# Optimization experiments

Hardware: AMD Instinct MI355X
Metric: run time of the kernel (lower is better)

Reference implementation:

```python
import jax, jax.numpy as jnp
import numpy as np

N_HEAD = 12

def setup_inputs() -> dict:
    key = jax.random.key(0)
    ks = jax.random.split(key, 5)
    B, T, C = 4, 2048, 768
    x = jax.random.normal(ks[0], (B, T, C), dtype=jnp.float32)
    s_in = 1.0 / np.sqrt(C)
    W_qkv = jax.random.normal(ks[1], (C, 3 * C), dtype=jnp.float32) * s_in
    b_qkv = jnp.zeros((3 * C,), dtype=jnp.float32)
    W_proj = jax.random.normal(ks[2], (C, C), dtype=jnp.float32) * s_in
    b_proj = jnp.zeros((C,), dtype=jnp.float32)
    return {"x": x, "W_qkv": W_qkv, "b_qkv": b_qkv, "W_proj": W_proj, "b_proj": b_proj}


def reference(x, W_qkv, b_qkv, W_proj, b_proj):
    B, T, C = x.shape
    H = N_HEAD
    D = C // H  # head dim
    qkv = x @ W_qkv + b_qkv                      # [B,T,3C]
    q, k, v = jnp.split(qkv, 3, axis=-1)
    # [B,T,C] -> [B,H,T,D]
    q = q.reshape(B, T, H, D).transpose(0, 2, 1, 3)
    k = k.reshape(B, T, H, D).transpose(0, 2, 1, 3)
    v = v.reshape(B, T, H, D).transpose(0, 2, 1, 3)
    att = jnp.einsum("bhqd,bhkd->bhqk", q, k) / jnp.sqrt(jnp.asarray(D, x.dtype))
    causal = jnp.tril(jnp.ones((T, T), dtype=bool))
    att = jnp.where(causal, att, jnp.asarray(-jnp.inf, att.dtype))
    att = jax.nn.softmax(att, axis=-1)
    y = jnp.einsum("bhqk,bhkd->bhqd", att, v)    # [B,H,T,D]
    y = y.transpose(0, 2, 1, 3).reshape(B, T, C)
    return y @ W_proj + b_proj
```

## Files before the change

### kernel.cpp

```cpp
#include <hip/hip_runtime.h>
#include <hip/hip_bf16.h>

typedef __bf16 bf16x8 __attribute__((ext_vector_type(8)));
typedef float f32x4 __attribute__((ext_vector_type(4)));
typedef unsigned int u32x4 __attribute__((ext_vector_type(4)));
typedef unsigned int u32x2 __attribute__((ext_vector_type(2)));
typedef int i32x2 __attribute__((ext_vector_type(2)));
typedef unsigned short u16;
typedef unsigned long long u64;

#define WAITVM(n) asm volatile("s_waitcnt vmcnt(" #n ")" ::: "memory")
#define SBAR() asm volatile("s_barrier" ::: "memory")

__device__ __forceinline__ u16 f2bf(float f) {
  unsigned u = __builtin_bit_cast(unsigned, f);
  u += 0x7FFFu + ((u >> 16) & 1u);
  return (u16)(u >> 16);
}
__device__ __forceinline__ unsigned cvtpk(float a, float b) {
  float2 f; f.x = a; f.y = b;
  __hip_bfloat162 h = __float22bfloat162_rn(f);
  unsigned u;
  __builtin_memcpy(&u, &h, 4);
  return u;
}

__device__ __forceinline__ void plswap(unsigned &a, unsigned &b) {
  i32x2 r = __builtin_amdgcn_permlane32_swap((int)a, (int)b, false, false);
  a = (unsigned)r[0];
  b = (unsigned)r[1];
}

__device__ __forceinline__ void gll16(const u16* g, u16* l) {
  __builtin_amdgcn_global_load_lds(
      (const __attribute__((address_space(1))) unsigned int*)g,
      (__attribute__((address_space(3))) unsigned int*)l, 16, 0, 0);
}

__global__ void cast_x_kernel(const float* __restrict__ in, u16* __restrict__ out, int n4) {
  int i = blockIdx.x * blockDim.x + threadIdx.x;
  if (i >= n4) return;
  f32x4 v = *(const f32x4*)(in + (size_t)i * 4);
  u32x2 pk;
  pk[0] = cvtpk(v[0], v[1]);
  pk[1] = cvtpk(v[2], v[3]);
  *(u32x2*)(out + (size_t)i * 4) = pk;
}

__global__ void transpose_cast_kernel(const float* __restrict__ W, u16* __restrict__ WT, int K, int N) {
  __shared__ float tile[32][33];
  int c0 = blockIdx.x * 32, r0 = blockIdx.y * 32;
  int tx = threadIdx.x & 31, tg = threadIdx.x >> 5;
#pragma unroll
  for (int i = 0; i < 4; ++i) {
    int r = tg + i * 8;
    tile[r][tx] = W[(size_t)(r0 + r) * N + c0 + tx];
  }
  __syncthreads();
#pragma unroll
  for (int i = 0; i < 4; ++i) {
    int r = tg + i * 8;
    WT[(size_t)(c0 + r) * K + r0 + tx] = f2bf(tile[tx][r]);
  }
}

__global__ __launch_bounds__(256, 4) void gemm_qkv_kernel(
    const u16* __restrict__ A, const u16* __restrict__ BT, const float* __restrict__ bias,
    u16* __restrict__ Qb, u16* __restrict__ Kb, u16* __restrict__ Vt) {
  constexpr int K = 768;
  constexpr int NS = K / 32;
  __shared__ u16 Asm[2][128 * 32];
  __shared__ u16 Bsm[2][128 * 32];
  const int tid = threadIdx.x;
  const int w = tid >> 6, lane = tid & 63;
  const int l15 = lane & 15, quad = lane >> 4;
  const int srow = tid >> 2, scol = (tid & 3) * 8;
  const int m0 = blockIdx.y * 128, n0 = blockIdx.x * 128;
  const u16* Ag = A + (size_t)(m0 + srow) * K + scol;
  const u16* Bg = BT + (size_t)(n0 + srow) * K + scol;
  const int mw = (w >> 1) * 64, nw = (w & 1) * 64;
  f32x4 acc[4][4];
#pragma unroll
  for (int i = 0; i < 4; ++i)
#pragma unroll
    for (int j = 0; j < 4; ++j) acc[i][j] = {0.f, 0.f, 0.f, 0.f};

  auto STAGE = [&](int buf, int ks) {
    const u16* a = Ag + ks * 32;
    const u16* b = Bg + ks * 32;
#pragma unroll
    for (int rb = 0; rb < 2; ++rb) {
      gll16(a + (size_t)rb * 64 * K, &Asm[buf][(rb * 64 + w * 16) * 32]);
      gll16(b + (size_t)rb * 64 * K, &Bsm[buf][(rb * 64 + w * 16) * 32]);
    }
  };
  auto COMPUTE = [&](int buf) {
    bf16x8 af[4], bfj[4];
#pragma unroll
    for (int i = 0; i < 4; ++i) af[i] = *(const bf16x8*)&Asm[buf][(mw + i * 16 + l15) * 32 + quad * 8];
#pragma unroll
    for (int j = 0; j < 4; ++j) bfj[j] = *(const bf16x8*)&Bsm[buf][(nw + j * 16 + l15) * 32 + quad * 8];
#pragma unroll
    for (int i = 0; i < 4; ++i)
#pragma unroll
      for (int j = 0; j < 4; ++j)
        acc[i][j] = __builtin_amdgcn_mfma_f32_16x16x32_bf16(af[i], bfj[j], acc[i][j], 0, 0, 0);
  };

  STAGE(0, 0);
  for (int s = 0; s + 2 < NS; s += 2) {
    STAGE(1, s + 1); WAITVM(4); SBAR(); COMPUTE(0); SBAR();
    STAGE(0, s + 2); WAITVM(4); SBAR(); COMPUTE(1); SBAR();
  }
  STAGE(1, NS - 1); WAITVM(4); SBAR(); COMPUTE(0);
  WAITVM(0); SBAR(); COMPUTE(1);

  const int sec = blockIdx.x / 6;
  const int nbase = n0 - sec * 768;
#pragma unroll
  for (int j = 0; j < 4; ++j) {
    const int nloc = nbase + nw + j * 16 + l15;
    const float bv = bias[sec * 768 + nloc];
    const int h = nloc >> 6, d = nloc & 63;
#pragma unroll
    for (int i = 0; i < 4; ++i) {
      const int m = m0 + mw + i * 16 + quad * 4;
      const int bb = m >> 11, trow = m & 2047;
      if (sec == 2) {
        u32x2 pk;
        pk[0] = cvtpk(acc[i][j][0] + bv, acc[i][j][1] + bv);
        pk[1] = cvtpk(acc[i][j][2] + bv, acc[i][j][3] + bv);
        *(u32x2*)(Vt + (size_t)((bb * 12 + h) * 64 + d) * 2048 + trow) = pk;
      } else {
        u16* dst = (sec == 0) ? Qb : Kb;
        const float scl = (sec == 0) ? 0.125f * 1.44269504f : 1.0f;
#pragma unroll
        for (int r = 0; r < 4; ++r)
          dst[(size_t)((bb * 12 + h) * 2048 + trow + r) * 64 + d] = f2bf((acc[i][j][r] + bv) * scl);
      }
    }
  }
}

__global__ __launch_bounds__(256, 4) void gemm_proj_kernel(
    const u16* __restrict__ A, const u16* __restrict__ BT, const float* __restrict__ bias,
    float* __restrict__ out) {
  constexpr int K = 768;
  constexpr int NS = K / 32;
  __shared__ u16 Asm[2][64 * 32];
  __shared__ u16 Bsm[2][128 * 32];
  const int tid = threadIdx.x;
  const int w = tid >> 6, lane = tid & 63;
  const int l15 = lane & 15, quad = lane >> 4;
  const int srow = tid >> 2, scol = (tid & 3) * 8;
  const int m0 = blockIdx.y * 64, n0 = blockIdx.x * 128;
  const u16* Ag = A + (size_t)(m0 + srow) * K + scol;
  const u16* Bg = BT + (size_t)(n0 + srow) * K + scol;
  const int mw = (w >> 1) * 32, nw = (w & 1) * 64;
  f32x4 acc[2][4];
#pragma unroll
  for (int i = 0; i < 2; ++i)
#pragma unroll
    for (int j = 0; j < 4; ++j) acc[i][j] = {0.f, 0.f, 0.f, 0.f};

  auto STAGE = [&](int buf, int ks) {
    const u16* a = Ag + ks * 32;
    const u16* b = Bg + ks * 32;
    gll16(a, &Asm[buf][(w * 16) * 32]);
#pragma unroll
    for (int rb = 0; rb < 2; ++rb)
      gll16(b + (size_t)rb * 64 * K, &Bsm[buf][(rb * 64 + w * 16) * 32]);
  };
  auto COMPUTE = [&](int buf) {
    bf16x8 af[2], bfj[4];
#pragma unroll
    for (int i = 0; i < 2; ++i) af[i] = *(const bf16x8*)&Asm[buf][(mw + i * 16 + l15) * 32 + quad * 8];
#pragma unroll
    for (int j = 0; j < 4; ++j) bfj[j] = *(const bf16x8*)&Bsm[buf][(nw + j * 16 + l15) * 32 + quad * 8];
#pragma unroll
    for (int i = 0; i < 2; ++i)
#pragma unroll
      for (int j = 0; j < 4; ++j)
        acc[i][j] = __builtin_amdgcn_mfma_f32_16x16x32_bf16(af[i], bfj[j], acc[i][j], 0, 0, 0);
  };

  STAGE(0, 0);
  for (int s = 0; s + 2 < NS; s += 2) {
    STAGE(1, s + 1); WAITVM(3); SBAR(); COMPUTE(0); SBAR();
    STAGE(0, s + 2); WAITVM(3); SBAR(); COMPUTE(1); SBAR();
  }
  STAGE(1, NS - 1); WAITVM(3); SBAR(); COMPUTE(0);
  WAITVM(0); SBAR(); COMPUTE(1);

#pragma unroll
  for (int j = 0; j < 4; ++j) {
    const int n = n0 + nw + j * 16 + l15;
    const float bv = bias[n];
#pragma unroll
    for (int i = 0; i < 2; ++i) {
      const int m = m0 + mw + i * 16 + quad * 4;
#pragma unroll
      for (int r = 0; r < 4; ++r) out[(size_t)(m + r) * 768 + n] = acc[i][j][r] + bv;
    }
  }
}

__global__ __launch_bounds__(256) void attn_split_kernel(
    const u16* __restrict__ Qg, const u16* __restrict__ Kg, const u16* __restrict__ Vtg,
    u16* __restrict__ Yb, float* __restrict__ Opart, float* __restrict__ lpart) {
  constexpr int T = 2048, D = 64;
  constexpr int LDP = 72;
  constexpr float MBOUND = 20.0f;
  __shared__ u16 Ks[2][64 * LDP];
  __shared__ u16 VTs[2][64 * LDP];
  const int s = 79 - blockIdx.x;
  const int bh = blockIdx.y;
  int qt, c;
  if (s < 8) { qt = s; c = 0; }
  else if (s < 24) { qt = 8 + ((s - 8) >> 1); c = (s - 8) & 1; }
  else if (s < 48) { int u = s - 24; int q3 = u / 3; qt = 16 + q3; c = u - 3 * q3; }
  else { int u = s - 48; qt = 24 + (u >> 2); c = u & 3; }
  const int niter = min(8, qt + 1 - 8 * c);
  const int tid = threadIdx.x;
  const int w = tid >> 6, lane = tid & 63;
  const int l15 = lane & 15, quad = lane >> 4;
  const int srow = tid >> 2, scol = (tid & 3) * 16;
  const u16* Kp = Kg + (size_t)bh * T * D;
  const u16* VTp = Vtg + (size_t)bh * D * T;

  const int qq = qt * 64 + w * 16 + l15;
  const u16* qrow = Qg + ((size_t)bh * T + qq) * D;
  const bf16x8 qfa = *(const bf16x8*)(qrow + quad * 8);
  const bf16x8 qfb = *(const bf16x8*)(qrow + 32 + quad * 8);

  u32x4 onesw; onesw[0] = 0x3F803F80u; onesw[1] = 0x3F803F80u; onesw[2] = 0x3F803F80u; onesw[3] = 0x3F803F80u;
  const bf16x8 ones = __builtin_bit_cast(bf16x8, onesw);

  f32x4 o[4] = {{0,0,0,0},{0,0,0,0},{0,0,0,0},{0,0,0,0}};
  f32x4 lacc = {0.f, 0.f, 0.f, 0.f};

  u32x4 kA, kB, vA, vB;
  auto LOADT = [&](int kt) {
    const int k1 = kt * 64;
    kA = *(const u32x4*)(Kp + (size_t)(k1 + srow) * D + scol);
    kB = *(const u32x4*)(Kp + (size_t)(k1 + srow) * D + scol + 8);
    vA = *(const u32x4*)(VTp + (size_t)srow * T + k1 + scol);
    vB = *(const u32x4*)(VTp + (size_t)srow * T + k1 + scol + 8);
  };
  auto STORET = [&](int buf) {
    *(u32x4*)&Ks[buf][srow * LDP + scol] = kA;
    *(u32x4*)&Ks[buf][srow * LDP + scol + 8] = kB;
    u32x2 t0; t0[0] = vA[0]; t0[1] = vA[1];
    u32x2 t1; t1[0] = vA[2]; t1[1] = vA[3];
    u32x2 t2; t2[0] = vB[0]; t2[1] = vB[1];
    u32x2 t3; t3[0] = vB[2]; t3[1] = vB[3];
    *(u32x2*)&VTs[buf][srow * LDP + scol] = t0;
    *(u32x2*)&VTs[buf][srow * LDP + scol + 8] = t1;
    *(u32x2*)&VTs[buf][srow * LDP + scol + 4] = t2;
    *(u32x2*)&VTs[buf][srow * LDP + scol + 12] = t3;
  };

  LOADT(c * 8);
  STORET(0);
  if (niter > 1) LOADT(c * 8 + 1);
  __syncthreads();

  for (int j = 0; j < niter; ++j) {
    const int buf = j & 1;
    const int ktg = c * 8 + j;
    f32x4 sA[4];
#pragma unroll
    for (int t = 0; t < 4; ++t) sA[t] = {-MBOUND, -MBOUND, -MBOUND, -MBOUND};
    __builtin_amdgcn_s_setprio(1);
#pragma unroll
    for (int t = 0; t < 4; ++t) {
      const bf16x8 kf0 = *(const bf16x8*)&Ks[buf][(t * 16 + l15) * LDP + quad * 8];
      const bf16x8 kf1 = *(const bf16x8*)&Ks[buf][(t * 16 + l15) * LDP + 32 + quad * 8];
      sA[t] = __builtin_amdgcn_mfma_f32_16x16x32_bf16(kf0, qfa, sA[t], 0, 0, 0);
      sA[t] = __builtin_amdgcn_mfma_f32_16x16x32_bf16(kf1, qfb, sA[t], 0, 0, 0);
    }
    __builtin_amdgcn_s_setprio(0);
    if (ktg == qt) {
      const int k0 = ktg * 64;
#pragma unroll
      for (int t = 0; t < 4; ++t)
#pragma unroll
        for (int r = 0; r < 4; ++r)
          if (k0 + t * 16 + quad * 4 + r > qq) sA[t][r] = -1e30f;
    }
    unsigned W[4][2];
#pragma unroll
    for (int t = 0; t < 4; ++t) {
      float e0 = __builtin_amdgcn_exp2f(sA[t][0]);
      float e1 = __builtin_amdgcn_exp2f(sA[t][1]);
      float e2 = __builtin_amdgcn_exp2f(sA[t][2]);
      float e3 = __builtin_amdgcn_exp2f(sA[t][3]);
      W[t][0] = cvtpk(e0, e1);
      W[t][1] = cvtpk(e2, e3);
    }
    plswap(W[0][0], W[1][0]);
    plswap(W[0][1], W[1][1]);
    plswap(W[2][0], W[3][0]);
    plswap(W[2][1], W[3][1]);
    u32x4 paw; paw[0] = W[0][0]; paw[1] = W[0][1]; paw[2] = W[1][0]; paw[3] = W[1][1];
    u32x4 pbw; pbw[0] = W[2][0]; pbw[1] = W[2][1]; pbw[2] = W[3][0]; pbw[3] = W[3][1];
    const bf16x8 pa = __builtin_bit_cast(bf16x8, paw);
    const bf16x8 pb = __builtin_bit_cast(bf16x8, pbw);
    __builtin_amdgcn_s_setprio(1);
    lacc = __builtin_amdgcn_mfma_f32_16x16x32_bf16(ones, pa, lacc, 0, 0, 0);
    lacc = __builtin_amdgcn_mfma_f32_16x16x32_bf16(ones, pb, lacc, 0, 0, 0);
#pragma unroll
    for (int t = 0; t < 4; ++t) {
      const bf16x8 vf0 = *(const bf16x8*)&VTs[buf][(t * 16 + l15) * LDP + quad * 8];
      const bf16x8 vf1 = *(const bf16x8*)&VTs[buf][(t * 16 + l15) * LDP + 32 + quad * 8];
      o[t] = __builtin_amdgcn_mfma_f32_16x16x32_bf16(vf0, pa, o[t], 0, 0, 0);
      o[t] = __builtin_amdgcn_mfma_f32_16x16x32_bf16(vf1, pb, o[t], 0, 0, 0);
    }
    __builtin_amdgcn_s_setprio(0);
    if (j + 1 < niter) {
      STORET(buf ^ 1);
      if (j + 2 < niter) LOADT(c * 8 + j + 2);
    }
    __syncthreads();
  }

  const float lv = lacc[0];
  if (qt <= 7) {
    const float inv = 1.f / lv;
    const int bidx = bh / 12, hidx = bh % 12;
    u16* y = Yb + ((size_t)bidx * T + qq) * 768 + hidx * 64;
#pragma unroll
    for (int t = 0; t < 4; ++t) {
      u32x2 pk;
      pk[0] = cvtpk(o[t][0] * inv, o[t][1] * inv);
      pk[1] = cvtpk(o[t][2] * inv, o[t][3] * inv);
      *(u32x2*)(y + t * 16 + quad * 4) = pk;
    }
  } else {
    const size_t pidx = (size_t)bh * 80 + s;
    float* Op = Opart + pidx * 4096 + (size_t)(w * 16 + l15) * 64;
#pragma unroll
    for (int t = 0; t < 4; ++t) *(f32x4*)(Op + t * 16 + quad * 4) = o[t];
    if (quad == 0) lpart[pidx * 64 + w * 16 + l15] = lv;
  }
}

__global__ __launch_bounds__(256) void attn_combine_kernel(
    const float* __restrict__ Opart, const float* __restrict__ lpart, u16* __restrict__ Yb) {
  constexpr int T = 2048;
  const int qt = 8 + blockIdx.x;
  const int bh = blockIdx.y;
  const int nch = (qt < 16) ? 2 : (qt < 24) ? 3 : 4;
  const int off = (qt < 16) ? 8 + (qt - 8) * 2 : (qt < 24) ? 24 + (qt - 16) * 3 : 48 + (qt - 24) * 4;
  const size_t base = (size_t)bh * 80 + off;
  const int tid = threadIdx.x;
  const int q = tid >> 2, db = (tid & 3) * 16;
  f32x4 o[4] = {{0,0,0,0},{0,0,0,0},{0,0,0,0},{0,0,0,0}};
  float l = 0.f;
  for (int cc = 0; cc < nch; ++cc) {
    const float* Op = Opart + (base + cc) * 4096 + (size_t)q * 64 + db;
#pragma unroll
    for (int v = 0; v < 4; ++v) o[v] += *(const f32x4*)(Op + v * 4);
    l += lpart[(base + cc) * 64 + q];
  }
  const float inv = 1.f / l;
  const int bidx = bh / 12, hidx = bh % 12;
  u16* y = Yb + ((size_t)bidx * T + qt * 64 + q) * 768 + hidx * 64 + db;
  u32x4 pk;
  pk[0] = cvtpk(o[0][0] * inv, o[0][1] * inv);
  pk[1] = cvtpk(o[0][2] * inv, o[0][3] * inv);
  pk[2] = cvtpk(o[1][0] * inv, o[1][1] * inv);
  pk[3] = cvtpk(o[1][2] * inv, o[1][3] * inv);
  *(u32x4*)y = pk;
  pk[0] = cvtpk(o[2][0] * inv, o[2][1] * inv);
  pk[1] = cvtpk(o[2][2] * inv, o[2][3] * inv);
  pk[2] = cvtpk(o[3][0] * inv, o[3][1] * inv);
  pk[3] = cvtpk(o[3][2] * inv, o[3][3] * inv);
  *(u32x4*)(y + 8) = pk;
}

__global__ __launch_bounds__(256) void attn_kernel(
    const u16* __restrict__ Qg, const u16* __restrict__ Kg, const u16* __restrict__ Vtg,
    u16* __restrict__ Yb) {
  constexpr int T = 2048, D = 64;
  constexpr int LDP = 72;
  constexpr float MBOUND = 20.0f;
  __shared__ u16 Ks[64 * LDP];
  __shared__ u16 VTs[64 * LDP];
  __shared__ u16 Ps[4 * 32 * LDP];
  const int qb = 15 - blockIdx.x;
  const int bh = blockIdx.y;
  const int Q0 = qb * 128;
  const int bidx = bh / 12, hidx = bh % 12;
  const int tid = threadIdx.x;
  const int w = tid >> 6, lane = tid & 63;
  const int l15 = lane & 15, quad = lane >> 4;
  const int srow = tid >> 2, scol = (tid & 3) * 16;
  const u16* Kp = Kg + (size_t)bh * T * D;
  const u16* VTp = Vtg + (size_t)bh * D * T;
  u16* pw0 = &Ps[(w * 32) * LDP];
  u16* pw1 = &Ps[(w * 32 + 16) * LDP];
  const u16* qrow0 = Qg + ((size_t)bh * T + Q0 + w * 16 + l15) * D;
  const bf16x8 qf0a = *(const bf16x8*)(qrow0 + quad * 8);
  const bf16x8 qf0b = *(const bf16x8*)(qrow0 + 32 + quad * 8);
  const bf16x8 qf1a = *(const bf16x8*)(qrow0 + (size_t)64 * D + quad * 8);
  const bf16x8 qf1b = *(const bf16x8*)(qrow0 + (size_t)64 * D + 32 + quad * 8);
  const int qq0 = Q0 + w * 16 + l15, qq1 = qq0 + 64;
  f32x4 o0[4] = {{0,0,0,0},{0,0,0,0},{0,0,0,0},{0,0,0,0}};
  f32x4 o1[4] = {{0,0,0,0},{0,0,0,0},{0,0,0,0},{0,0,0,0}};
  float l0v = 0.f, l1v = 0.f;
  const int nkt = 2 * qb + 2;
  u32x4 kA = *(const u32x4*)(Kp + (size_t)srow * D + scol);
  u32x4 kB = *(const u32x4*)(Kp + (size_t)srow * D + scol + 8);
  u32x4 vA = *(const u32x4*)(VTp + (size_t)srow * T + scol);
  u32x4 vB = *(const u32x4*)(VTp + (size_t)srow * T + scol + 8);
  for (int kt = 0; kt < nkt; ++kt) {
    __syncthreads();
    *(u32x4*)&Ks[srow * LDP + scol] = kA;
    *(u32x4*)&Ks[srow * LDP + scol + 8] = kB;
    *(u32x4*)&VTs[srow * LDP + scol] = vA;
    *(u32x4*)&VTs[srow * LDP + scol + 8] = vB;
    __syncthreads();
    if (kt + 1 < nkt) {
      const int k1 = (kt + 1) * 64;
      kA = *(const u32x4*)(Kp + (size_t)(k1 + srow) * D + scol);
      kB = *(const u32x4*)(Kp + (size_t)(k1 + srow) * D + scol + 8);
      vA = *(const u32x4*)(VTp + (size_t)srow * T + k1 + scol);
      vB = *(const u32x4*)(VTp + (size_t)srow * T + k1 + scol + 8);
    }
    const int k0 = kt * 64;
    const bool g0a = (kt <= 2 * qb);
    f32x4 s0[4] = {{0,0,0,0},{0,0,0,0},{0,0,0,0},{0,0,0,0}};
    f32x4 s1[4] = {{0,0,0,0},{0,0,0,0},{0,0,0,0},{0,0,0,0}};
#pragma unroll
    for (int t = 0; t < 4; ++t) {
      const bf16x8 kf0 = *(const bf16x8*)&Ks[(t * 16 + l15) * LDP + quad * 8];
      const bf16x8 kf1 = *(const bf16x8*)&Ks[(t * 16 + l15) * LDP + 32 + quad * 8];
      s0[t] = __builtin_amdgcn_mfma_f32_16x16x32_bf16(kf0, qf0a, s0[t], 0, 0, 0);
      s0[t] = __builtin_amdgcn_mfma_f32_16x16x32_bf16(kf1, qf0b, s0[t], 0, 0, 0);
      s1[t] = __builtin_amdgcn_mfma_f32_16x16x32_bf16(kf0, qf1a, s1[t], 0, 0, 0);
      s1[t] = __builtin_amdgcn_mfma_f32_16x16x32_bf16(kf1, qf1b, s1[t], 0, 0, 0);
    }
    if (g0a) {
      if (kt == 2 * qb) {
#pragma unroll
        for (int t = 0; t < 4; ++t)
#pragma unroll
          for (int r = 0; r < 4; ++r)
            if (k0 + t * 16 + quad * 4 + r > qq0) s0[t][r] = -1e30f;
      }
#pragma unroll
      for (int t = 0; t < 4; ++t) {
        float e0 = __builtin_amdgcn_exp2f(s0[t][0] - MBOUND);
        float e1 = __builtin_amdgcn_exp2f(s0[t][1] - MBOUND);
        float e2 = __builtin_amdgcn_exp2f(s0[t][2] - MBOUND);
        float e3 = __builtin_amdgcn_exp2f(s0[t][3] - MBOUND);
        l0v += (e0 + e1) + (e2 + e3);
        u32x2 pk;
        pk[0] = cvtpk(e0, e1);
        pk[1] = cvtpk(e2, e3);
        *(u32x2*)&pw0[l15 * LDP + t * 16 + quad * 4] = pk;
      }
    }
    {
      if (kt == 2 * qb + 1) {
#pragma unroll
        for (int t = 0; t < 4; ++t)
#pragma unroll
          for (int r = 0; r < 4; ++r)
            if (k0 + t * 16 + quad * 4 + r > qq1) s1[t][r] = -1e30f;
      }
#pragma unroll
      for (int t = 0; t < 4; ++t) {
        float e0 = __builtin_amdgcn_exp2f(s1[t][0] - MBOUND);
        float e1 = __builtin_amdgcn_exp2f(s1[t][1] - MBOUND);
        float e2 = __builtin_amdgcn_exp2f(s1[t][2] - MBOUND);
        float e3 = __builtin_amdgcn_exp2f(s1[t][3] - MBOUND);
        l1v += (e0 + e1) + (e2 + e3);
        u32x2 pk;
        pk[0] = cvtpk(e0, e1);
        pk[1] = cvtpk(e2, e3);
        *(u32x2*)&pw1[l15 * LDP + t * 16 + quad * 4] = pk;
      }
    }
    const bf16x8 p0a = *(const bf16x8*)&pw0[l15 * LDP + quad * 8];
    const bf16x8 p0b = *(const bf16x8*)&pw0[l15 * LDP + 32 + quad * 8];
    const bf16x8 p1a = *(const bf16x8*)&pw1[l15 * LDP + quad * 8];
    const bf16x8 p1b = *(const bf16x8*)&pw1[l15 * LDP + 32 + quad * 8];
#pragma unroll
    for (int t = 0; t < 4; ++t) {
      const bf16x8 vf0 = *(const bf16x8*)&VTs[(t * 16 + l15) * LDP + quad * 8];
      const bf16x8 vf1 = *(const bf16x8*)&VTs[(t * 16 + l15) * LDP + 32 + quad * 8];
      if (g0a) {
        o0[t] = __builtin_amdgcn_mfma_f32_16x16x32_bf16(vf0, p0a, o0[t], 0, 0, 0);
        o0[t] = __builtin_amdgcn_mfma_f32_16x16x32_bf16(vf1, p0b, o0[t], 0, 0, 0);
      }
      o1[t] = __builtin_amdgcn_mfma_f32_16x16x32_bf16(vf0, p1a, o1[t], 0, 0, 0);
      o1[t] = __builtin_amdgcn_mfma_f32_16x16x32_bf16(vf1, p1b, o1[t], 0, 0, 0);
    }
  }
  l0v += __shfl_xor(l0v, 16); l0v += __shfl_xor(l0v, 32);
  l1v += __shfl_xor(l1v, 16); l1v += __shfl_xor(l1v, 32);
  const float inv0 = 1.f / l0v, inv1 = 1.f / l1v;
  u16* y0 = Yb + ((size_t)bidx * T + qq0) * 768 + hidx * 64;
  u16* y1 = Yb + ((size_t)bidx * T + qq1) * 768 + hidx * 64;
#pragma unroll
  for (int t = 0; t < 4; ++t) {
    u32x2 pk0, pk1;
    pk0[0] = cvtpk(o0[t][0] * inv0, o0[t][1] * inv0);
    pk0[1] = cvtpk(o0[t][2] * inv0, o0[t][3] * inv0);
    pk1[0] = cvtpk(o1[t][0] * inv1, o1[t][1] * inv1);
    pk1[1] = cvtpk(o1[t][2] * inv1, o1[t][3] * inv1);
    *(u32x2*)(y0 + t * 16 + quad * 4) = pk0;
    *(u32x2*)(y1 + t * 16 + quad * 4) = pk1;
  }
}

extern "C" void kernel_launch(void* const* d_in, const int* in_sizes, int n_in,
                              void* d_out, int out_size, void* d_ws, size_t ws_size,
                              hipStream_t stream) {
  const float* x = (const float*)d_in[0];
  const float* W_qkv = (const float*)d_in[1];
  const float* b_qkv = (const float*)d_in[2];
  const float* W_proj = (const float*)d_in[3];
  const float* b_proj = (const float*)d_in[4];
  float* out = (float*)d_out;

  constexpr size_t MC = (size_t)8192 * 768;
  u16* xb = (u16*)d_ws;
  u16* Qb = xb + MC;
  u16* Kb = Qb + MC;
  u16* Vt = Kb + MC;
  u16* Yb = Vt + MC;
  u16* WqkvT = Yb + MC;
  u16* WprojT = WqkvT + (size_t)2304 * 768;
  constexpr size_t BASE_U16 = 5 * MC + (size_t)2304 * 768 + (size_t)768 * 768;
  float* Opart = (float*)((u16*)d_ws + BASE_U16);
  float* lpart = Opart + (size_t)3840 * 4096;
  constexpr size_t NEED = BASE_U16 * 2 + ((size_t)3840 * 4096 + (size_t)3840 * 64) * 4;
  const bool use_split = (ws_size >= NEED);

  cast_x_kernel<<<6291456 / (4 * 256), 256, 0, stream>>>(x, xb, 6291456 / 4);
  transpose_cast_kernel<<<dim3(2304 / 32, 768 / 32), 256, 0, stream>>>(W_qkv, WqkvT, 768, 2304);
  transpose_cast_kernel<<<dim3(768 / 32, 768 / 32), 256, 0, stream>>>(W_proj, WprojT, 768, 768);
  gemm_qkv_kernel<<<dim3(18, 64), 256, 0, stream>>>(xb, WqkvT, b_qkv, Qb, Kb, Vt);
  if (use_split) {
    attn_split_kernel<<<dim3(80, 48), 256, 0, stream>>>(Qb, Kb, Vt, Yb, Opart, lpart);
    attn_combine_kernel<<<dim3(24, 48), 256, 0, stream>>>(Opart, lpart, Yb);
  } else {
    attn_kernel<<<dim3(16, 48), 256, 0, stream>>>(Qb, Kb, Vt, Yb);
  }
  gemm_proj_kernel<<<dim3(6, 128), 256, 0, stream>>>(Yb, WprojT, b_proj, out);
}
```

Measured before the change: 227.4 us.

## Double split-attention query tile to 128 rows with 512-thread blocks sharing K/V tiles

Each split-attention block now covers 128 query rows with 8 waves instead of 64 rows with 4 waves. Every K/V tile staged in LDS is therefore reused by twice as many query rows, halving global K/V traffic and block count. Waves in the lower half of the tile skip the extra diagonal key tile, and the partial-output layout and combine kernel are resized to match. The trade-off is fewer, larger blocks, some idle waves on the diagonal iteration, and coarser load balance.

```diff
diff --git a/kernel.cpp b/kernel.cpp
--- a/kernel.cpp
+++ b/kernel.cpp
@@ -205,7 +205,7 @@
   }
 }
 
-__global__ __launch_bounds__(256) void attn_split_kernel(
+__global__ __launch_bounds__(512) void attn_split_kernel(
     const u16* __restrict__ Qg, const u16* __restrict__ Kg, const u16* __restrict__ Vtg,
     u16* __restrict__ Yb, float* __restrict__ Opart, float* __restrict__ lpart) {
   constexpr int T = 2048, D = 64;
@@ -213,22 +213,27 @@
   constexpr float MBOUND = 20.0f;
   __shared__ u16 Ks[2][64 * LDP];
   __shared__ u16 VTs[2][64 * LDP];
-  const int s = 79 - blockIdx.x;
+  const int s = 39 - blockIdx.x;
   const int bh = blockIdx.y;
-  int qt, c;
-  if (s < 8) { qt = s; c = 0; }
-  else if (s < 24) { qt = 8 + ((s - 8) >> 1); c = (s - 8) & 1; }
-  else if (s < 48) { int u = s - 24; int q3 = u / 3; qt = 16 + q3; c = u - 3 * q3; }
-  else { int u = s - 48; qt = 24 + (u >> 2); c = u & 3; }
-  const int niter = min(8, qt + 1 - 8 * c);
+  int qt2, c;
+  if (s < 4) { qt2 = s; c = 0; }
+  else if (s < 12) { qt2 = 4 + ((s - 4) >> 1); c = (s - 4) & 1; }
+  else if (s < 24) { int u = s - 12; int q3 = u / 3; qt2 = 8 + q3; c = u - 3 * q3; }
+  else { int u = s - 24; qt2 = 12 + (u >> 2); c = u & 3; }
+  const int nkt = 2 * qt2 + 2;
+  const int niter = min(8, nkt - 8 * c);
   const int tid = threadIdx.x;
   const int w = tid >> 6, lane = tid & 63;
   const int l15 = lane & 15, quad = lane >> 4;
-  const int srow = tid >> 2, scol = (tid & 3) * 16;
+  const int srow = tid >> 3;
+  const int scol = (tid & 7) * 8;
+  const int so0 = scol - 4 * (tid & 1);
+  const int so1 = scol + 8 - 4 * (tid & 1);
   const u16* Kp = Kg + (size_t)bh * T * D;
   const u16* VTp = Vtg + (size_t)bh * D * T;
 
-  const int qq = qt * 64 + w * 16 + l15;
+  const int wdiag = 2 * qt2 + (w >> 2);
+  const int qq = qt2 * 128 + w * 16 + l15;
   const u16* qrow = Qg + ((size_t)bh * T + qq) * D;
   const bf16x8 qfa = *(const bf16x8*)(qrow + quad * 8);
   const bf16x8 qfb = *(const bf16x8*)(qrow + 32 + quad * 8);
@@ -239,25 +244,18 @@
   f32x4 o[4] = {{0,0,0,0},{0,0,0,0},{0,0,0,0},{0,0,0,0}};
   f32x4 lacc = {0.f, 0.f, 0.f, 0.f};
 
-  u32x4 kA, kB, vA, vB;
+  u32x4 kA, vA;
   auto LOADT = [&](int kt) {
     const int k1 = kt * 64;
     kA = *(const u32x4*)(Kp + (size_t)(k1 + srow) * D + scol);
-    kB = *(const u32x4*)(Kp + (size_t)(k1 + srow) * D + scol + 8);
     vA = *(const u32x4*)(VTp + (size_t)srow * T + k1 + scol);
-    vB = *(const u32x4*)(VTp + (size_t)srow * T + k1 + scol + 8);
   };
   auto STORET = [&](int buf) {
     *(u32x4*)&Ks[buf][srow * LDP + scol] = kA;
-    *(u32x4*)&Ks[buf][srow * LDP + scol + 8] = kB;
-    u32x2 t0; t0[0] = vA[0]; t0[1] = vA[1];
-    u32x2 t1; t1[0] = vA[2]; t1[1] = vA[3];
-    u32x2 t2; t2[0] = vB[0]; t2[1] = vB[1];
-    u32x2 t3; t3[0] = vB[2]; t3[1] = vB[3];
-    *(u32x2*)&VTs[buf][srow * LDP + scol] = t0;
-    *(u32x2*)&VTs[buf][srow * LDP + scol + 8] = t1;
-    *(u32x2*)&VTs[buf][srow * LDP + scol + 4] = t2;
-    *(u32x2*)&VTs[buf][srow * LDP + scol + 12] = t3;
+    u32x2 vlo; vlo[0] = vA[0]; vlo[1] = vA[1];
+    u32x2 vhi; vhi[0] = vA[2]; vhi[1] = vA[3];
+    *(u32x2*)&VTs[buf][srow * LDP + so0] = vlo;
+    *(u32x2*)&VTs[buf][srow * LDP + so1] = vhi;
   };
 
   LOADT(c * 8);
@@ -268,55 +266,57 @@
   for (int j = 0; j < niter; ++j) {
     const int buf = j & 1;
     const int ktg = c * 8 + j;
-    f32x4 sA[4];
-#pragma unroll
-    for (int t = 0; t < 4; ++t) sA[t] = {-MBOUND, -MBOUND, -MBOUND, -MBOUND};
-    __builtin_amdgcn_s_setprio(1);
-#pragma unroll
-    for (int t = 0; t < 4; ++t) {
-      const bf16x8 kf0 = *(const bf16x8*)&Ks[buf][(t * 16 + l15) * LDP + quad * 8];
-      const bf16x8 kf1 = *(const bf16x8*)&Ks[buf][(t * 16 + l15) * LDP + 32 + quad * 8];
-      sA[t] = __builtin_amdgcn_mfma_f32_16x16x32_bf16(kf0, qfa, sA[t], 0, 0, 0);
-      sA[t] = __builtin_amdgcn_mfma_f32_16x16x32_bf16(kf1, qfb, sA[t], 0, 0, 0);
-    }
-    __builtin_amdgcn_s_setprio(0);
-    if (ktg == qt) {
-      const int k0 = ktg * 64;
-#pragma unroll
-      for (int t = 0; t < 4; ++t)
-#pragma unroll
-        for (int r = 0; r < 4; ++r)
-          if (k0 + t * 16 + quad * 4 + r > qq) sA[t][r] = -1e30f;
-    }
-    unsigned W[4][2];
-#pragma unroll
-    for (int t = 0; t < 4; ++t) {
-      float e0 = __builtin_amdgcn_exp2f(sA[t][0]);
-      float e1 = __builtin_amdgcn_exp2f(sA[t][1]);
-      float e2 = __builtin_amdgcn_exp2f(sA[t][2]);
-      float e3 = __builtin_amdgcn_exp2f(sA[t][3]);
-      W[t][0] = cvtpk(e0, e1);
-      W[t][1] = cvtpk(e2, e3);
-    }
-    plswap(W[0][0], W[1][0]);
-    plswap(W[0][1], W[1][1]);
-    plswap(W[2][0], W[3][0]);
-    plswap(W[2][1], W[3][1]);
-    u32x4 paw; paw[0] = W[0][0]; paw[1] = W[0][1]; paw[2] = W[1][0]; paw[3] = W[1][1];
-    u32x4 pbw; pbw[0] = W[2][0]; pbw[1] = W[2][1]; pbw[2] = W[3][0]; pbw[3] = W[3][1];
-    const bf16x8 pa = __builtin_bit_cast(bf16x8, paw);
-    const bf16x8 pb = __builtin_bit_cast(bf16x8, pbw);
-    __builtin_amdgcn_s_setprio(1);
-    lacc = __builtin_amdgcn_mfma_f32_16x16x32_bf16(ones, pa, lacc, 0, 0, 0);
-    lacc = __builtin_amdgcn_mfma_f32_16x16x32_bf16(ones, pb, lacc, 0, 0, 0);
-#pragma unroll
-    for (int t = 0; t < 4; ++t) {
-      const bf16x8 vf0 = *(const bf16x8*)&VTs[buf][(t * 16 + l15) * LDP + quad * 8];
-      const bf16x8 vf1 = *(const bf16x8*)&VTs[buf][(t * 16 + l15) * LDP + 32 + quad * 8];
-      o[t] = __builtin_amdgcn_mfma_f32_16x16x32_bf16(vf0, pa, o[t], 0, 0, 0);
-      o[t] = __builtin_amdgcn_mfma_f32_16x16x32_bf16(vf1, pb, o[t], 0, 0, 0);
-    }
-    __builtin_amdgcn_s_setprio(0);
+    if (ktg <= wdiag) {
+      f32x4 sA[4];
+#pragma unroll
+      for (int t = 0; t < 4; ++t) sA[t] = {-MBOUND, -MBOUND, -MBOUND, -MBOUND};
+      __builtin_amdgcn_s_setprio(1);
+#pragma unroll
+      for (int t = 0; t < 4; ++t) {
+        const bf16x8 kf0 = *(const bf16x8*)&Ks[buf][(t * 16 + l15) * LDP + quad * 8];
+        const bf16x8 kf1 = *(const bf16x8*)&Ks[buf][(t * 16 + l15) * LDP + 32 + quad * 8];
+        sA[t] = __builtin_amdgcn_mfma_f32_16x16x32_bf16(kf0, qfa, sA[t], 0, 0, 0);
+        sA[t] = __builtin_amdgcn_mfma_f32_16x16x32_bf16(kf1, qfb, sA[t], 0, 0, 0);
+      }
+      __builtin_amdgcn_s_setprio(0);
+      if (ktg == wdiag) {
+        const int k0 = ktg * 64;
+#pragma unroll
+        for (int t = 0; t < 4; ++t)
+#pragma unroll
+          for (int r = 0; r < 4; ++r)
+            if (k0 + t * 16 + quad * 4 + r > qq) sA[t][r] = -1e30f;
+      }
+      unsigned W[4][2];
+#pragma unroll
+      for (int t = 0; t < 4; ++t) {
+        float e0 = __builtin_amdgcn_exp2f(sA[t][0]);
+        float e1 = __builtin_amdgcn_exp2f(sA[t][1]);
+        float e2 = __builtin_amdgcn_exp2f(sA[t][2]);
+        float e3 = __builtin_amdgcn_exp2f(sA[t][3]);
+        W[t][0] = cvtpk(e0, e1);
+        W[t][1] = cvtpk(e2, e3);
+      }
+      plswap(W[0][0], W[1][0]);
+      plswap(W[0][1], W[1][1]);
+      plswap(W[2][0], W[3][0]);
+      plswap(W[2][1], W[3][1]);
+      u32x4 paw; paw[0] = W[0][0]; paw[1] = W[0][1]; paw[2] = W[1][0]; paw[3] = W[1][1];
+      u32x4 pbw; pbw[0] = W[2][0]; pbw[1] = W[2][1]; pbw[2] = W[3][0]; pbw[3] = W[3][1];
+      const bf16x8 pa = __builtin_bit_cast(bf16x8, paw);
+      const bf16x8 pb = __builtin_bit_cast(bf16x8, pbw);
+      __builtin_amdgcn_s_setprio(1);
+      lacc = __builtin_amdgcn_mfma_f32_16x16x32_bf16(ones, pa, lacc, 0, 0, 0);
+      lacc = __builtin_amdgcn_mfma_f32_16x16x32_bf16(ones, pb, lacc, 0, 0, 0);
+#pragma unroll
+      for (int t = 0; t < 4; ++t) {
+        const bf16x8 vf0 = *(const bf16x8*)&VTs[buf][(t * 16 + l15) * LDP + quad * 8];
+        const bf16x8 vf1 = *(const bf16x8*)&VTs[buf][(t * 16 + l15) * LDP + 32 + quad * 8];
+        o[t] = __builtin_amdgcn_mfma_f32_16x16x32_bf16(vf0, pa, o[t], 0, 0, 0);
+        o[t] = __builtin_amdgcn_mfma_f32_16x16x32_bf16(vf1, pb, o[t], 0, 0, 0);
+      }
+      __builtin_amdgcn_s_setprio(0);
+    }
     if (j + 1 < niter) {
       STORET(buf ^ 1);
       if (j + 2 < niter) LOADT(c * 8 + j + 2);
@@ -325,7 +325,7 @@
   }
 
   const float lv = lacc[0];
-  if (qt <= 7) {
+  if (qt2 <= 3) {
     const float inv = 1.f / lv;
     const int bidx = bh / 12, hidx = bh % 12;
     u16* y = Yb + ((size_t)bidx * T + qq) * 768 + hidx * 64;
@@ -337,46 +337,49 @@
       *(u32x2*)(y + t * 16 + quad * 4) = pk;
     }
   } else {
-    const size_t pidx = (size_t)bh * 80 + s;
-    float* Op = Opart + pidx * 4096 + (size_t)(w * 16 + l15) * 64;
+    const size_t pidx = (size_t)bh * 40 + s;
+    float* Op = Opart + pidx * 8192 + (size_t)(w * 16 + l15) * 64;
 #pragma unroll
     for (int t = 0; t < 4; ++t) *(f32x4*)(Op + t * 16 + quad * 4) = o[t];
-    if (quad == 0) lpart[pidx * 64 + w * 16 + l15] = lv;
+    if (quad == 0) lpart[pidx * 128 + w * 16 + l15] = lv;
   }
 }
 
 __global__ __launch_bounds__(256) void attn_combine_kernel(
     const float* __restrict__ Opart, const float* __restrict__ lpart, u16* __restrict__ Yb) {
   constexpr int T = 2048;
-  const int qt = 8 + blockIdx.x;
+  const int qt2 = 4 + blockIdx.x;
   const int bh = blockIdx.y;
-  const int nch = (qt < 16) ? 2 : (qt < 24) ? 3 : 4;
-  const int off = (qt < 16) ? 8 + (qt - 8) * 2 : (qt < 24) ? 24 + (qt - 16) * 3 : 48 + (qt - 24) * 4;
-  const size_t base = (size_t)bh * 80 + off;
+  const int nch = (qt2 < 8) ? 2 : (qt2 < 12) ? 3 : 4;
+  const int off = (qt2 < 8) ? 4 + (qt2 - 4) * 2 : (qt2 < 12) ? 12 + (qt2 - 8) * 3 : 24 + (qt2 - 12) * 4;
+  const size_t base = (size_t)bh * 40 + off;
   const int tid = threadIdx.x;
-  const int q = tid >> 2, db = (tid & 3) * 16;
-  f32x4 o[4] = {{0,0,0,0},{0,0,0,0},{0,0,0,0},{0,0,0,0}};
+  const int q = tid >> 1, db = (tid & 1) * 32;
+  f32x4 o[8] = {{0,0,0,0},{0,0,0,0},{0,0,0,0},{0,0,0,0},{0,0,0,0},{0,0,0,0},{0,0,0,0},{0,0,0,0}};
   float l = 0.f;
   for (int cc = 0; cc < nch; ++cc) {
-    const float* Op = Opart + (base + cc) * 4096 + (size_t)q * 64 + db;
-#pragma unroll
-    for (int v = 0; v < 4; ++v) o[v] += *(const f32x4*)(Op + v * 4);
-    l += lpart[(base + cc) * 64 + q];
+    const float* Op = Opart + (base + cc) * 8192 + (size_t)q * 64 + db;
+#pragma unroll
+    for (int v = 0; v < 8; ++v) o[v] += *(const f32x4*)(Op + v * 4);
+    l += lpart[(base + cc) * 128 + q];
   }
   const float inv = 1.f / l;
   const int bidx = bh / 12, hidx = bh % 12;
-  u16* y = Yb + ((size_t)bidx * T + qt * 64 + q) * 768 + hidx * 64 + db;
-  u32x4 pk;
-  pk[0] = cvtpk(o[0][0] * inv, o[0][1] * inv);
-  pk[1] = cvtpk(o[0][2] * inv, o[0][3] * inv);
-  pk[2] = cvtpk(o[1][0] * inv, o[1][1] * inv);
-  pk[3] = cvtpk(o[1][2] * inv, o[1][3] * inv);
-  *(u32x4*)y = pk;
-  pk[0] = cvtpk(o[2][0] * inv, o[2][1] * inv);
-  pk[1] = cvtpk(o[2][2] * inv, o[2][3] * inv);
-  pk[2] = cvtpk(o[3][0] * inv, o[3][1] * inv);
-  pk[3] = cvtpk(o[3][2] * inv, o[3][3] * inv);
-  *(u32x4*)(y + 8) = pk;
+  u16* y = Yb + ((size_t)bidx * T + qt2 * 128 + q) * 768 + hidx * 64 + db;
+#pragma unroll
+  for (int g = 0; g < 2; ++g) {
+    u32x4 pk;
+    pk[0] = cvtpk(o[g * 4 + 0][0] * inv, o[g * 4 + 0][1] * inv);
+    pk[1] = cvtpk(o[g * 4 + 0][2] * inv, o[g * 4 + 0][3] * inv);
+    pk[2] = cvtpk(o[g * 4 + 1][0] * inv, o[g * 4 + 1][1] * inv);
+    pk[3] = cvtpk(o[g * 4 + 1][2] * inv, o[g * 4 + 1][3] * inv);
+    *(u32x4*)(y + g * 16) = pk;
+    pk[0] = cvtpk(o[g * 4 + 2][0] * inv, o[g * 4 + 2][1] * inv);
+    pk[1] = cvtpk(o[g * 4 + 2][2] * inv, o[g * 4 + 2][3] * inv);
+    pk[2] = cvtpk(o[g * 4 + 3][0] * inv, o[g * 4 + 3][1] * inv);
+    pk[3] = cvtpk(o[g * 4 + 3][2] * inv, o[g * 4 + 3][3] * inv);
+    *(u32x4*)(y + g * 16 + 8) = pk;
+  }
 }
 
 __global__ __launch_bounds__(256) void attn_kernel(
@@ -536,8 +539,8 @@
   u16* WprojT = WqkvT + (size_t)2304 * 768;
   constexpr size_t BASE_U16 = 5 * MC + (size_t)2304 * 768 + (size_t)768 * 768;
   float* Opart = (float*)((u16*)d_ws + BASE_U16);
-  float* lpart = Opart + (size_t)3840 * 4096;
-  constexpr size_t NEED = BASE_U16 * 2 + ((size_t)3840 * 4096 + (size_t)3840 * 64) * 4;
+  float* lpart = Opart + (size_t)1920 * 8192;
+  constexpr size_t NEED = BASE_U16 * 2 + ((size_t)1920 * 8192 + (size_t)1920 * 128) * 4;
   const bool use_split = (ws_size >= NEED);
 
   cast_x_kernel<<<6291456 / (4 * 256), 256, 0, stream>>>(x, xb, 6291456 / 4);
@@ -545,8 +548,8 @@
   transpose_cast_kernel<<<dim3(768 / 32, 768 / 32), 256, 0, stream>>>(W_proj, WprojT, 768, 768);
   gemm_qkv_kernel<<<dim3(18, 64), 256, 0, stream>>>(xb, WqkvT, b_qkv, Qb, Kb, Vt);
   if (use_split) {
-    attn_split_kernel<<<dim3(80, 48), 256, 0, stream>>>(Qb, Kb, Vt, Yb, Opart, lpart);
-    attn_combine_kernel<<<dim3(24, 48), 256, 0, stream>>>(Opart, lpart, Yb);
+    attn_split_kernel<<<dim3(40, 48), 512, 0, stream>>>(Qb, Kb, Vt, Yb, Opart, lpart);
+    attn_combine_kernel<<<dim3(12, 48), 256, 0, stream>>>(Opart, lpart, Yb);
   } else {
     attn_kernel<<<dim3(16, 48), 256, 0, stream>>>(Qb, Kb, Vt, Yb);
   }
```

After: 230.7 us. About the same (+1.5%).
